# Performance work log

Hardware: AMD Instinct MI355X
Metric: run time of the kernel (lower is better)

The kernel has to match this reference:

```python
import jax, jax.numpy as jnp
import numpy as np

L, B, D, H, LAYERS = 512, 256, 512, 512, 2


def setup_inputs() -> dict:
    key = jax.random.key(0)
    ks = jax.random.split(key, 7)
    s = 0.05  # small init scale for stable recurrence
    return {
        "carry": jnp.zeros((B, LAYERS * H), jnp.float32),
        "x": jax.random.normal(ks[0], (L, B, D), jnp.float32),
        "Wi0": jax.random.normal(ks[1], (D, 3 * H), jnp.float32) * s,
        "Wh0": jax.random.normal(ks[2], (H, 3 * H), jnp.float32) * s,
        "bh0": jnp.zeros((3 * H,), jnp.float32),
        "Wi1": jax.random.normal(ks[3], (H, 3 * H), jnp.float32) * s,
        "Wh1": jax.random.normal(ks[4], (H, 3 * H), jnp.float32) * s,
        "bh1": jnp.zeros((3 * H,), jnp.float32),
    }


def _gru_cell(h, xin, Wi, Wh, bh):
    # flax.linen.GRUCell math: input-side Dense has no bias, hidden-side Dense has bias.
    gi = xin @ Wi            # [B, 3H] -> (ir, iz, in)
    gh = h @ Wh + bh         # [B, 3H] -> (hr, hz, hn)
    ir, iz, inn = jnp.split(gi, 3, axis=-1)
    hr, hz, hn = jnp.split(gh, 3, axis=-1)
    r = jax.nn.sigmoid(ir + hr)
    z = jax.nn.sigmoid(iz + hz)
    n = jnp.tanh(inn + r * hn)
    return (1.0 - z) * n + z * h


def reference(carry, x, Wi0, Wh0, bh0, Wi1, Wh1, bh1):
    params = ((Wi0, Wh0, bh0), (Wi1, Wh1, bh1))

    def step(c, xt):
        hs = jnp.split(c, LAYERS, axis=-1)  # per-layer hidden states
        inp = xt
        new_hs = []
        for i, (Wi, Wh, bh) in enumerate(params):  # fixed small layer loop
            h = _gru_cell(hs[i], inp, Wi, Wh, bh)
            new_hs.append(h)
            inp = h  # output of layer i feeds layer i+1
        return jnp.concatenate(new_hs, axis=-1), inp

    carry, y = jax.lax.scan(step, carry, x)  # y: [L, B, H]
    return carry, y
```

## Files before the change

### kernel.cpp

```cpp
#include <hip/hip_runtime.h>


#define LSEQ 512
#define TH3 1536

#define WT_OFF   0
#define H0_OFF   6291456
#define H1_OFF   6815744
#define BAR_OFF  7340032

typedef _Float16 f16x8 __attribute__((ext_vector_type(8)));
typedef float f32x4 __attribute__((ext_vector_type(4)));

__device__ __forceinline__ float sig_(float v) { return 1.0f / (1.0f + __expf(-v)); }
__device__ __forceinline__ float tanh_(float v) { return 2.0f / (1.0f + __expf(-2.0f * v)) - 1.0f; }

__device__ __forceinline__ f32x4 load16_bypass(const void* p) {
  f32x4 r;
  asm volatile("global_load_dwordx4 %0, %1, off sc0 sc1" : "=v"(r) : "v"(p));
  return r;
}
__device__ __forceinline__ void store2_bypass(_Float16* p, _Float16 v) {
  asm volatile("global_store_short %0, %1, off sc0 sc1" :: "v"(p), "v"(v) : "memory");
}

__global__ void prep_kernel(const float* __restrict__ Wh0, const float* __restrict__ Wi1,
                            const float* __restrict__ Wh1, const float* __restrict__ Wi0,
                            char* __restrict__ ws) {
  const int b = blockIdx.x;
  const int w = b >> 9;
  const int k = b & 511;
  const float* src = (w == 0) ? Wh0 : (w == 1) ? Wi1 : (w == 2) ? Wh1 : Wi0;
  _Float16* dst = (_Float16*)(ws + WT_OFF);
  const int kc = k >> 5;
  const int lthi = ((k >> 3) & 3) << 4;
  const int e = k & 7;
  for (int col = threadIdx.x; col < TH3; col += 256) {
    float v = src[(size_t)k * TH3 + col];
    int nt = col >> 9, c = col & 511, cid = c >> 4, j = c & 15;
    size_t idx = (size_t)(w * 32 + cid) * 24576 + (size_t)((kc * 3 + nt) * 64 + lthi + j) * 8 + e;
    dst[idx] = (_Float16)v;
  }
  if (b == 0) {
    unsigned int* bar = (unsigned int*)(ws + BAR_OFF);
    for (int i = threadIdx.x; i < 512; i += 256) bar[i] = 0u;
  }
}

__device__ __forceinline__ void group_barrier(unsigned int* bar) {
  __syncthreads();
  if (threadIdx.x == 0) {
    unsigned int my = __hip_atomic_load(bar + 1, __ATOMIC_RELAXED, __HIP_MEMORY_SCOPE_AGENT);
    unsigned int prev = __hip_atomic_fetch_add(bar, 1u, __ATOMIC_RELAXED, __HIP_MEMORY_SCOPE_AGENT);
    if (prev == 31u) {
      __hip_atomic_store(bar, 0u, __ATOMIC_RELAXED, __HIP_MEMORY_SCOPE_AGENT);
      __hip_atomic_fetch_add(bar + 1, 1u, __ATOMIC_RELAXED, __HIP_MEMORY_SCOPE_AGENT);
    } else {
      while (__hip_atomic_load(bar + 1, __ATOMIC_RELAXED, __HIP_MEMORY_SCOPE_AGENT) == my) {
      }
    }
  }
  __syncthreads();
}

__global__ void __launch_bounds__(512, 2)
gru_kernel(const float* __restrict__ carry, const float* __restrict__ x,
           const float* __restrict__ bh0, const float* __restrict__ bh1,
           float* __restrict__ out, char* __restrict__ ws) {
  extern __shared__ char smem[];
  _Float16* Wlds = (_Float16*)smem;
  float* GH = (float*)(smem + 147456);

  const int bid = blockIdx.x;
  const int g = bid & 7, cid = bid >> 3;
  const int tid = threadIdx.x;
  const int wid = tid >> 6, lane = tid & 63;
  const int l16 = lane & 15, lhi = lane >> 4;
  const int mhalf = wid & 1, role = wid >> 1;

  _Float16* wt = (_Float16*)(ws + WT_OFF);
  _Float16* h0buf = (_Float16*)(ws + H0_OFF) + (size_t)g * 32768;
  _Float16* h1buf = (_Float16*)(ws + H1_OFF) + (size_t)g * 32768;
  unsigned int* bar = (unsigned int*)(ws + BAR_OFF) + g * 64;

  for (int w = 0; w < 3; ++w) {
    const f16x8* s8 = (const f16x8*)(wt + (size_t)(w * 32 + cid) * 24576);
    f16x8* d8 = (f16x8*)(Wlds + w * 24576);
    for (int i = tid; i < 3072; i += 512) d8[i] = s8[i];
  }

  const int hcol = cid * 16 + l16;
  const int rowq0 = mhalf * 16 + 4 * lhi;

  float bR = 0.f, bZ = 0.f, bN = 0.f;
  f32x4 hst = {0.f, 0.f, 0.f, 0.f};
  if (role == 1 || role == 2) {
    const float* bh = (role == 1) ? bh0 : bh1;
    bR = bh[hcol]; bZ = bh[512 + hcol]; bN = bh[1024 + hcol];
    const int loff = (role == 1) ? 0 : 512;
    _Float16* hb = (role == 1) ? h0buf : h1buf;
#pragma unroll
    for (int q = 0; q < 4; ++q) {
      float h = carry[(size_t)(g * 32 + rowq0 + q) * 1024 + loff + hcol];
      hst[q] = h;
      store2_bypass(&hb[16384 + (rowq0 + q) * 512 + hcol], (_Float16)h);
    }
    asm volatile("s_waitcnt vmcnt(0)" ::: "memory");
  }
  group_barrier(bar);

  const f16x8* Wb0 = (const f16x8*)Wlds;
  const f16x8* Wb1 = (const f16x8*)(Wlds + 24576);
  const f16x8* Wb2 = (const f16x8*)(Wlds + 2 * 24576);
  const f16x8* WbX = (const f16x8*)(wt + (size_t)(3 * 32 + cid) * 24576);

  for (int s = 0; s <= LSEQ; ++s) {
    const int pr = (s + 1) & 1;
    const int pw = s & 1;
    f32x4 a0 = {0.f, 0.f, 0.f, 0.f}, a1 = {0.f, 0.f, 0.f, 0.f}, a2 = {0.f, 0.f, 0.f, 0.f};

    if (role == 0 && s < LSEQ) {
      const _Float16* Ap = h0buf + pr * 16384 + (mhalf * 16 + l16) * 512 + 8 * lhi;
      f16x8 afr[16];
#pragma unroll
      for (int kc = 0; kc < 16; ++kc) afr[kc] = __builtin_bit_cast(f16x8, load16_bypass(Ap + kc * 32));
      asm volatile("s_waitcnt vmcnt(0)" ::: "memory");
      __builtin_amdgcn_sched_barrier(0);
#pragma unroll
      for (int kc = 0; kc < 16; ++kc) {
        a0 = __builtin_amdgcn_mfma_f32_16x16x32_f16(afr[kc], Wb0[(kc * 3 + 0) * 64 + lane], a0, 0, 0, 0);
        a1 = __builtin_amdgcn_mfma_f32_16x16x32_f16(afr[kc], Wb0[(kc * 3 + 1) * 64 + lane], a1, 0, 0, 0);
        a2 = __builtin_amdgcn_mfma_f32_16x16x32_f16(afr[kc], Wb0[(kc * 3 + 2) * 64 + lane], a2, 0, 0, 0);
      }
#pragma unroll
      for (int q = 0; q < 4; ++q) {
        GH[(0 * 32 + rowq0 + q) * 16 + l16] = a0[q];
        GH[(1 * 32 + rowq0 + q) * 16 + l16] = a1[q];
        GH[(2 * 32 + rowq0 + q) * 16 + l16] = a2[q];
      }
    } else if (role == 3 && s >= 1) {
      const _Float16* Ap = h1buf + pw * 16384 + (mhalf * 16 + l16) * 512 + 8 * lhi;
      f16x8 afr[16];
#pragma unroll
      for (int kc = 0; kc < 16; ++kc) afr[kc] = __builtin_bit_cast(f16x8, load16_bypass(Ap + kc * 32));
      asm volatile("s_waitcnt vmcnt(0)" ::: "memory");
      __builtin_amdgcn_sched_barrier(0);
#pragma unroll
      for (int kc = 0; kc < 16; ++kc) {
        a0 = __builtin_amdgcn_mfma_f32_16x16x32_f16(afr[kc], Wb2[(kc * 3 + 0) * 64 + lane], a0, 0, 0, 0);
        a1 = __builtin_amdgcn_mfma_f32_16x16x32_f16(afr[kc], Wb2[(kc * 3 + 1) * 64 + lane], a1, 0, 0, 0);
        a2 = __builtin_amdgcn_mfma_f32_16x16x32_f16(afr[kc], Wb2[(kc * 3 + 2) * 64 + lane], a2, 0, 0, 0);
      }
#pragma unroll
      for (int q = 0; q < 4; ++q) {
        GH[((3 + 0) * 32 + rowq0 + q) * 16 + l16] = a0[q];
        GH[((3 + 1) * 32 + rowq0 + q) * 16 + l16] = a1[q];
        GH[((3 + 2) * 32 + rowq0 + q) * 16 + l16] = a2[q];
      }
    } else if (role == 1 && s < LSEQ) {
      const float* xp = x + ((size_t)s * 256 + g * 32 + mhalf * 16 + l16) * 512 + 8 * lhi;
#pragma unroll
      for (int kc = 0; kc < 16; ++kc) {
        f32x4 xa = *(const f32x4*)(xp + kc * 32);
        f32x4 xb = *(const f32x4*)(xp + kc * 32 + 4);
        f16x8 a;
        a[0] = (_Float16)xa[0]; a[1] = (_Float16)xa[1]; a[2] = (_Float16)xa[2]; a[3] = (_Float16)xa[3];
        a[4] = (_Float16)xb[0]; a[5] = (_Float16)xb[1]; a[6] = (_Float16)xb[2]; a[7] = (_Float16)xb[3];
        a0 = __builtin_amdgcn_mfma_f32_16x16x32_f16(a, WbX[(kc * 3 + 0) * 64 + lane], a0, 0, 0, 0);
        a1 = __builtin_amdgcn_mfma_f32_16x16x32_f16(a, WbX[(kc * 3 + 1) * 64 + lane], a1, 0, 0, 0);
        a2 = __builtin_amdgcn_mfma_f32_16x16x32_f16(a, WbX[(kc * 3 + 2) * 64 + lane], a2, 0, 0, 0);
      }
    } else if (role == 2 && s >= 1) {
      const _Float16* Ap = h0buf + pr * 16384 + (mhalf * 16 + l16) * 512 + 8 * lhi;
      f16x8 afr[16];
#pragma unroll
      for (int kc = 0; kc < 16; ++kc) afr[kc] = __builtin_bit_cast(f16x8, load16_bypass(Ap + kc * 32));
      asm volatile("s_waitcnt vmcnt(0)" ::: "memory");
      __builtin_amdgcn_sched_barrier(0);
#pragma unroll
      for (int kc = 0; kc < 16; ++kc) {
        a0 = __builtin_amdgcn_mfma_f32_16x16x32_f16(afr[kc], Wb1[(kc * 3 + 0) * 64 + lane], a0, 0, 0, 0);
        a1 = __builtin_amdgcn_mfma_f32_16x16x32_f16(afr[kc], Wb1[(kc * 3 + 1) * 64 + lane], a1, 0, 0, 0);
        a2 = __builtin_amdgcn_mfma_f32_16x16x32_f16(afr[kc], Wb1[(kc * 3 + 2) * 64 + lane], a2, 0, 0, 0);
      }
    }
    __syncthreads();

    if (role == 1 && s < LSEQ) {
#pragma unroll
      for (int q = 0; q < 4; ++q) {
        const int row = rowq0 + q;
        float r = sig_(a0[q] + GH[(0 * 32 + row) * 16 + l16] + bR);
        float z = sig_(a1[q] + GH[(1 * 32 + row) * 16 + l16] + bZ);
        float n = tanh_(a2[q] + r * (GH[(2 * 32 + row) * 16 + l16] + bN));
        float h = (1.0f - z) * n + z * hst[q];
        hst[q] = h;
        store2_bypass(&h0buf[pw * 16384 + row * 512 + hcol], (_Float16)h);
        if (s == LSEQ - 1) out[(size_t)(g * 32 + row) * 1024 + hcol] = h;
      }
      asm volatile("s_waitcnt vmcnt(0)" ::: "memory");
    } else if (role == 2 && s >= 1) {
#pragma unroll
      for (int q = 0; q < 4; ++q) {
        const int row = rowq0 + q;
        float r = sig_(a0[q] + GH[((3 + 0) * 32 + row) * 16 + l16] + bR);
        float z = sig_(a1[q] + GH[((3 + 1) * 32 + row) * 16 + l16] + bZ);
        float n = tanh_(a2[q] + r * (GH[((3 + 2) * 32 + row) * 16 + l16] + bN));
        float h = (1.0f - z) * n + z * hst[q];
        hst[q] = h;
        store2_bypass(&h1buf[pr * 16384 + row * 512 + hcol], (_Float16)h);
        out[(size_t)262144 + ((size_t)(s - 1) * 256 + g * 32 + row) * 512 + hcol] = h;
        if (s == LSEQ) out[(size_t)(g * 32 + row) * 1024 + 512 + hcol] = h;
      }
      asm volatile("s_waitcnt vmcnt(0)" ::: "memory");
    }
    group_barrier(bar);
  }
}

extern "C" void kernel_launch(void* const* d_in, const int* in_sizes, int n_in,
                              void* d_out, int out_size, void* d_ws, size_t ws_size,
                              hipStream_t stream) {
  const float* carry = (const float*)d_in[0];
  const float* x     = (const float*)d_in[1];
  const float* Wi0   = (const float*)d_in[2];
  const float* Wh0   = (const float*)d_in[3];
  const float* bh0   = (const float*)d_in[4];
  const float* Wi1   = (const float*)d_in[5];
  const float* Wh1   = (const float*)d_in[6];
  const float* bh1   = (const float*)d_in[7];
  float* out = (float*)d_out;
  char* ws = (char*)d_ws;

  prep_kernel<<<2048, 256, 0, stream>>>(Wh0, Wi1, Wh1, Wi0, ws);

  (void)hipFuncSetAttribute(reinterpret_cast<const void*>(gru_kernel),
                            hipFuncAttributeMaxDynamicSharedMemorySize, 159744);

  void* args[] = {(void*)&carry, (void*)&x, (void*)&bh0, (void*)&bh1, (void*)&out, (void*)&ws};
  (void)hipLaunchCooperativeKernel(reinterpret_cast<void*>(gru_kernel),
                                   dim3(256), dim3(512), args, 159744, stream);
}
```

Measured before the change: 9.717 ms.

## Map batch groups to XCCs at runtime so h-exchange can stay in L2

Each block reads its hardware XCC id and takes a rank within that XCC through atomics, so every batch group of 32 blocks lands on one XCC. When the mapping is valid, the hidden-state loads and stores drop the sc1 bit and can be served from the XCC-local L2 instead of bypassing to memory. If the mapping check fails, the kernel falls back to the old block-index mapping with full bypass. The group barrier is also simplified to a monotonically increasing counter. This adds a two-phase global startup barrier across all 256 blocks, which relies on every block being co-resident.

```diff
diff --git a/kernel.cpp b/kernel.cpp
--- a/kernel.cpp
+++ b/kernel.cpp
@@ -8,6 +8,9 @@
 #define H0_OFF   6291456
 #define H1_OFF   6815744
 #define BAR_OFF  7340032
+#define RANK_OFF 7342080
+#define GBAR_OFF 7344128
+#define BAD_OFF  7344384
 
 typedef _Float16 f16x8 __attribute__((ext_vector_type(8)));
 typedef float f32x4 __attribute__((ext_vector_type(4)));
@@ -15,13 +18,17 @@
 __device__ __forceinline__ float sig_(float v) { return 1.0f / (1.0f + __expf(-v)); }
 __device__ __forceinline__ float tanh_(float v) { return 2.0f / (1.0f + __expf(-2.0f * v)) - 1.0f; }
 
-__device__ __forceinline__ f32x4 load16_bypass(const void* p) {
+template <bool FAST>
+__device__ __forceinline__ f32x4 load16h(const void* p) {
   f32x4 r;
-  asm volatile("global_load_dwordx4 %0, %1, off sc0 sc1" : "=v"(r) : "v"(p));
+  if (FAST) asm volatile("global_load_dwordx4 %0, %1, off sc0" : "=v"(r) : "v"(p));
+  else      asm volatile("global_load_dwordx4 %0, %1, off sc0 sc1" : "=v"(r) : "v"(p));
   return r;
 }
-__device__ __forceinline__ void store2_bypass(_Float16* p, _Float16 v) {
-  asm volatile("global_store_short %0, %1, off sc0 sc1" :: "v"(p), "v"(v) : "memory");
+template <bool FAST>
+__device__ __forceinline__ void store2h(_Float16* p, _Float16 v) {
+  if (FAST) asm volatile("global_store_short %0, %1, off sc0" :: "v"(p), "v"(v) : "memory");
+  else      asm volatile("global_store_short %0, %1, off sc0 sc1" :: "v"(p), "v"(v) : "memory");
 }
 
 __global__ void prep_kernel(const float* __restrict__ Wh0, const float* __restrict__ Wi1,
@@ -42,37 +49,24 @@
     dst[idx] = (_Float16)v;
   }
   if (b == 0) {
-    unsigned int* bar = (unsigned int*)(ws + BAR_OFF);
-    for (int i = threadIdx.x; i < 512; i += 256) bar[i] = 0u;
-  }
-}
-
-__device__ __forceinline__ void group_barrier(unsigned int* bar) {
+    unsigned int* z = (unsigned int*)(ws + BAR_OFF);
+    for (int i = threadIdx.x; i < 1152; i += 256) z[i] = 0u;
+  }
+}
+
+__device__ __forceinline__ void group_barrier(unsigned int* barp, unsigned int target, int tid) {
   __syncthreads();
-  if (threadIdx.x == 0) {
-    unsigned int my = __hip_atomic_load(bar + 1, __ATOMIC_RELAXED, __HIP_MEMORY_SCOPE_AGENT);
-    unsigned int prev = __hip_atomic_fetch_add(bar, 1u, __ATOMIC_RELAXED, __HIP_MEMORY_SCOPE_AGENT);
-    if (prev == 31u) {
-      __hip_atomic_store(bar, 0u, __ATOMIC_RELAXED, __HIP_MEMORY_SCOPE_AGENT);
-      __hip_atomic_fetch_add(bar + 1, 1u, __ATOMIC_RELAXED, __HIP_MEMORY_SCOPE_AGENT);
-    } else {
-      while (__hip_atomic_load(bar + 1, __ATOMIC_RELAXED, __HIP_MEMORY_SCOPE_AGENT) == my) {
-      }
-    }
+  if (tid == 0) {
+    __hip_atomic_fetch_add(barp, 1u, __ATOMIC_RELAXED, __HIP_MEMORY_SCOPE_AGENT);
+    while (__hip_atomic_load(barp, __ATOMIC_RELAXED, __HIP_MEMORY_SCOPE_AGENT) < target) {}
   }
   __syncthreads();
 }
 
-__global__ void __launch_bounds__(512, 2)
-gru_kernel(const float* __restrict__ carry, const float* __restrict__ x,
-           const float* __restrict__ bh0, const float* __restrict__ bh1,
-           float* __restrict__ out, char* __restrict__ ws) {
-  extern __shared__ char smem[];
-  _Float16* Wlds = (_Float16*)smem;
-  float* GH = (float*)(smem + 147456);
-
-  const int bid = blockIdx.x;
-  const int g = bid & 7, cid = bid >> 3;
+template <bool FAST>
+__device__ __forceinline__ void run_scan(int g, int cid, const float* carry, const float* x,
+                                         const float* bh0, const float* bh1, float* out,
+                                         char* ws, _Float16* Wlds, float* GH) {
   const int tid = threadIdx.x;
   const int wid = tid >> 6, lane = tid & 63;
   const int l16 = lane & 15, lhi = lane >> 4;
@@ -81,13 +75,8 @@
   _Float16* wt = (_Float16*)(ws + WT_OFF);
   _Float16* h0buf = (_Float16*)(ws + H0_OFF) + (size_t)g * 32768;
   _Float16* h1buf = (_Float16*)(ws + H1_OFF) + (size_t)g * 32768;
-  unsigned int* bar = (unsigned int*)(ws + BAR_OFF) + g * 64;
-
-  for (int w = 0; w < 3; ++w) {
-    const f16x8* s8 = (const f16x8*)(wt + (size_t)(w * 32 + cid) * 24576);
-    f16x8* d8 = (f16x8*)(Wlds + w * 24576);
-    for (int i = tid; i < 3072; i += 512) d8[i] = s8[i];
-  }
+  unsigned int* barp = (unsigned int*)(ws + BAR_OFF) + g * 64;
+  unsigned int phase = 0;
 
   const int hcol = cid * 16 + l16;
   const int rowq0 = mhalf * 16 + 4 * lhi;
@@ -103,11 +92,11 @@
     for (int q = 0; q < 4; ++q) {
       float h = carry[(size_t)(g * 32 + rowq0 + q) * 1024 + loff + hcol];
       hst[q] = h;
-      store2_bypass(&hb[16384 + (rowq0 + q) * 512 + hcol], (_Float16)h);
+      store2h<FAST>(&hb[16384 + (rowq0 + q) * 512 + hcol], (_Float16)h);
     }
     asm volatile("s_waitcnt vmcnt(0)" ::: "memory");
   }
-  group_barrier(bar);
+  group_barrier(barp, 32u * (++phase), tid);
 
   const f16x8* Wb0 = (const f16x8*)Wlds;
   const f16x8* Wb1 = (const f16x8*)(Wlds + 24576);
@@ -123,7 +112,7 @@
       const _Float16* Ap = h0buf + pr * 16384 + (mhalf * 16 + l16) * 512 + 8 * lhi;
       f16x8 afr[16];
 #pragma unroll
-      for (int kc = 0; kc < 16; ++kc) afr[kc] = __builtin_bit_cast(f16x8, load16_bypass(Ap + kc * 32));
+      for (int kc = 0; kc < 16; ++kc) afr[kc] = __builtin_bit_cast(f16x8, load16h<FAST>(Ap + kc * 32));
       asm volatile("s_waitcnt vmcnt(0)" ::: "memory");
       __builtin_amdgcn_sched_barrier(0);
 #pragma unroll
@@ -142,7 +131,7 @@
       const _Float16* Ap = h1buf + pw * 16384 + (mhalf * 16 + l16) * 512 + 8 * lhi;
       f16x8 afr[16];
 #pragma unroll
-      for (int kc = 0; kc < 16; ++kc) afr[kc] = __builtin_bit_cast(f16x8, load16_bypass(Ap + kc * 32));
+      for (int kc = 0; kc < 16; ++kc) afr[kc] = __builtin_bit_cast(f16x8, load16h<FAST>(Ap + kc * 32));
       asm volatile("s_waitcnt vmcnt(0)" ::: "memory");
       __builtin_amdgcn_sched_barrier(0);
 #pragma unroll
@@ -174,7 +163,7 @@
       const _Float16* Ap = h0buf + pr * 16384 + (mhalf * 16 + l16) * 512 + 8 * lhi;
       f16x8 afr[16];
 #pragma unroll
-      for (int kc = 0; kc < 16; ++kc) afr[kc] = __builtin_bit_cast(f16x8, load16_bypass(Ap + kc * 32));
+      for (int kc = 0; kc < 16; ++kc) afr[kc] = __builtin_bit_cast(f16x8, load16h<FAST>(Ap + kc * 32));
       asm volatile("s_waitcnt vmcnt(0)" ::: "memory");
       __builtin_amdgcn_sched_barrier(0);
 #pragma unroll
@@ -195,7 +184,7 @@
         float n = tanh_(a2[q] + r * (GH[(2 * 32 + row) * 16 + l16] + bN));
         float h = (1.0f - z) * n + z * hst[q];
         hst[q] = h;
-        store2_bypass(&h0buf[pw * 16384 + row * 512 + hcol], (_Float16)h);
+        store2h<FAST>(&h0buf[pw * 16384 + row * 512 + hcol], (_Float16)h);
         if (s == LSEQ - 1) out[(size_t)(g * 32 + row) * 1024 + hcol] = h;
       }
       asm volatile("s_waitcnt vmcnt(0)" ::: "memory");
@@ -208,14 +197,61 @@
         float n = tanh_(a2[q] + r * (GH[((3 + 2) * 32 + row) * 16 + l16] + bN));
         float h = (1.0f - z) * n + z * hst[q];
         hst[q] = h;
-        store2_bypass(&h1buf[pr * 16384 + row * 512 + hcol], (_Float16)h);
+        store2h<FAST>(&h1buf[pr * 16384 + row * 512 + hcol], (_Float16)h);
         out[(size_t)262144 + ((size_t)(s - 1) * 256 + g * 32 + row) * 512 + hcol] = h;
         if (s == LSEQ) out[(size_t)(g * 32 + row) * 1024 + 512 + hcol] = h;
       }
       asm volatile("s_waitcnt vmcnt(0)" ::: "memory");
     }
-    group_barrier(bar);
-  }
+    group_barrier(barp, 32u * (++phase), tid);
+  }
+}
+
+__global__ void __launch_bounds__(512, 2)
+gru_kernel(const float* __restrict__ carry, const float* __restrict__ x,
+           const float* __restrict__ bh0, const float* __restrict__ bh1,
+           float* __restrict__ out, char* __restrict__ ws) {
+  extern __shared__ char smem[];
+  _Float16* Wlds = (_Float16*)smem;
+  float* GH = (float*)(smem + 147456);
+  __shared__ int sh_g, sh_cid, sh_fast;
+
+  const int tid = threadIdx.x;
+
+  if (tid == 0) {
+    unsigned int xcc;
+    asm volatile("s_getreg_b32 %0, hwreg(HW_REG_XCC_ID)" : "=s"(xcc));
+    xcc &= 7u;
+    unsigned int* rk = (unsigned int*)(ws + RANK_OFF) + xcc * 64;
+    unsigned int* gb = (unsigned int*)(ws + GBAR_OFF);
+    unsigned int* bd = (unsigned int*)(ws + BAD_OFF);
+    unsigned int cid_raw = __hip_atomic_fetch_add(rk, 1u, __ATOMIC_RELAXED, __HIP_MEMORY_SCOPE_AGENT);
+    asm volatile("s_waitcnt vmcnt(0)" ::: "memory");
+    __hip_atomic_fetch_add(gb, 1u, __ATOMIC_RELAXED, __HIP_MEMORY_SCOPE_AGENT);
+    while (__hip_atomic_load(gb, __ATOMIC_RELAXED, __HIP_MEMORY_SCOPE_AGENT) < 256u) {}
+    unsigned int cnt = __hip_atomic_load(rk, __ATOMIC_RELAXED, __HIP_MEMORY_SCOPE_AGENT);
+    if (cnt != 32u || cid_raw >= 32u)
+      __hip_atomic_fetch_add(bd, 1u, __ATOMIC_RELAXED, __HIP_MEMORY_SCOPE_AGENT);
+    asm volatile("s_waitcnt vmcnt(0)" ::: "memory");
+    __hip_atomic_fetch_add(gb, 1u, __ATOMIC_RELAXED, __HIP_MEMORY_SCOPE_AGENT);
+    while (__hip_atomic_load(gb, __ATOMIC_RELAXED, __HIP_MEMORY_SCOPE_AGENT) < 512u) {}
+    unsigned int badv = __hip_atomic_load(bd, __ATOMIC_RELAXED, __HIP_MEMORY_SCOPE_AGENT);
+    sh_fast = (badv == 0u);
+    sh_g    = (badv == 0u) ? (int)xcc     : (int)(blockIdx.x & 7);
+    sh_cid  = (badv == 0u) ? (int)cid_raw : (int)(blockIdx.x >> 3);
+  }
+  __syncthreads();
+  const int g = sh_g, cid = sh_cid;
+
+  _Float16* wt = (_Float16*)(ws + WT_OFF);
+  for (int w = 0; w < 3; ++w) {
+    const f16x8* s8 = (const f16x8*)(wt + (size_t)(w * 32 + cid) * 24576);
+    f16x8* d8 = (f16x8*)(Wlds + w * 24576);
+    for (int i = tid; i < 3072; i += 512) d8[i] = s8[i];
+  }
+
+  if (sh_fast) run_scan<true>(g, cid, carry, x, bh0, bh1, out, ws, Wlds, GH);
+  else         run_scan<false>(g, cid, carry, x, bh0, bh1, out, ws, Wlds, GH);
 }
 
 extern "C" void kernel_launch(void* const* d_in, const int* in_sizes, int n_in,
```

New measurement: 8.616 ms. 11.3% less time.

## Replace per-step group barrier with per-wave dataflow flags and LDS handoffs

Applied to the files above, without the earlier changes.

Removes the block-wide __syncthreads plus single-thread atomic group barrier that ran every timestep. Each wave role now runs its own loop and synchronises through per-wave global flags, polled with a 64-lane ballot, and LDS release/acquire counters. This lets layer-0 and layer-1 work and the x-projection run ahead of each other instead of moving in lockstep. The cost is more global polling traffic and a subtle memory-ordering protocol that relies on relaxed atomics and cache-bypass stores being visible across blocks.

```diff
diff --git a/kernel.cpp b/kernel.cpp
--- a/kernel.cpp
+++ b/kernel.cpp
@@ -7,7 +7,8 @@
 #define WT_OFF   0
 #define H0_OFF   6291456
 #define H1_OFF   6815744
-#define BAR_OFF  7340032
+#define F0_OFF   7340032
+#define F1_OFF   7405568
 
 typedef _Float16 f16x8 __attribute__((ext_vector_type(8)));
 typedef float f32x4 __attribute__((ext_vector_type(4)));
@@ -15,13 +16,30 @@
 __device__ __forceinline__ float sig_(float v) { return 1.0f / (1.0f + __expf(-v)); }
 __device__ __forceinline__ float tanh_(float v) { return 2.0f / (1.0f + __expf(-2.0f * v)) - 1.0f; }
 
-__device__ __forceinline__ f32x4 load16_bypass(const void* p) {
+__device__ __forceinline__ f32x4 load16b(const void* p) {
   f32x4 r;
   asm volatile("global_load_dwordx4 %0, %1, off sc0 sc1" : "=v"(r) : "v"(p));
   return r;
 }
-__device__ __forceinline__ void store2_bypass(_Float16* p, _Float16 v) {
+__device__ __forceinline__ void store2b(_Float16* p, _Float16 v) {
   asm volatile("global_store_short %0, %1, off sc0 sc1" :: "v"(p), "v"(v) : "memory");
+}
+
+__device__ __forceinline__ void astore(unsigned int* p, unsigned int v) {
+  __hip_atomic_store(p, v, __ATOMIC_RELAXED, __HIP_MEMORY_SCOPE_AGENT);
+}
+__device__ __forceinline__ unsigned int aload(unsigned int* p) {
+  return __hip_atomic_load(p, __ATOMIC_RELAXED, __HIP_MEMORY_SCOPE_AGENT);
+}
+__device__ __forceinline__ void poll64(char* base, int lane, unsigned int target) {
+  unsigned int* p = (unsigned int*)(base + lane * 128);
+  while (__ballot(aload(p) >= target) != ~0ull) {}
+}
+__device__ __forceinline__ void lds_post(unsigned int* f, unsigned int v) {
+  __hip_atomic_store(f, v, __ATOMIC_RELEASE, __HIP_MEMORY_SCOPE_WORKGROUP);
+}
+__device__ __forceinline__ void lds_poll(unsigned int* f, unsigned int v) {
+  while (__hip_atomic_load(f, __ATOMIC_ACQUIRE, __HIP_MEMORY_SCOPE_WORKGROUP) < v) {}
 }
 
 __global__ void prep_kernel(const float* __restrict__ Wh0, const float* __restrict__ Wi1,
@@ -42,25 +60,9 @@
     dst[idx] = (_Float16)v;
   }
   if (b == 0) {
-    unsigned int* bar = (unsigned int*)(ws + BAR_OFF);
-    for (int i = threadIdx.x; i < 512; i += 256) bar[i] = 0u;
-  }
-}
-
-__device__ __forceinline__ void group_barrier(unsigned int* bar) {
-  __syncthreads();
-  if (threadIdx.x == 0) {
-    unsigned int my = __hip_atomic_load(bar + 1, __ATOMIC_RELAXED, __HIP_MEMORY_SCOPE_AGENT);
-    unsigned int prev = __hip_atomic_fetch_add(bar, 1u, __ATOMIC_RELAXED, __HIP_MEMORY_SCOPE_AGENT);
-    if (prev == 31u) {
-      __hip_atomic_store(bar, 0u, __ATOMIC_RELAXED, __HIP_MEMORY_SCOPE_AGENT);
-      __hip_atomic_fetch_add(bar + 1, 1u, __ATOMIC_RELAXED, __HIP_MEMORY_SCOPE_AGENT);
-    } else {
-      while (__hip_atomic_load(bar + 1, __ATOMIC_RELAXED, __HIP_MEMORY_SCOPE_AGENT) == my) {
-      }
-    }
-  }
-  __syncthreads();
+    unsigned int* z = (unsigned int*)(ws + F0_OFF);
+    for (int i = threadIdx.x; i < 32768; i += 256) z[i] = 0u;
+  }
 }
 
 __global__ void __launch_bounds__(512, 2)
@@ -69,152 +71,197 @@
            float* __restrict__ out, char* __restrict__ ws) {
   extern __shared__ char smem[];
   _Float16* Wlds = (_Float16*)smem;
-  float* GH = (float*)(smem + 147456);
-
-  const int bid = blockIdx.x;
-  const int g = bid & 7, cid = bid >> 3;
+  float* gi0buf = (float*)(smem + 147456);
+  float* gh1buf = (float*)(smem + 153600);
+  __shared__ unsigned int sf[8];
+
   const int tid = threadIdx.x;
   const int wid = tid >> 6, lane = tid & 63;
   const int l16 = lane & 15, lhi = lane >> 4;
   const int mhalf = wid & 1, role = wid >> 1;
+  const int g = blockIdx.x & 7, cid = blockIdx.x >> 3;
+
+  if (tid < 8) sf[tid] = 0u;
 
   _Float16* wt = (_Float16*)(ws + WT_OFF);
   _Float16* h0buf = (_Float16*)(ws + H0_OFF) + (size_t)g * 32768;
   _Float16* h1buf = (_Float16*)(ws + H1_OFF) + (size_t)g * 32768;
-  unsigned int* bar = (unsigned int*)(ws + BAR_OFF) + g * 64;
+  char* f0g = ws + F0_OFF + (size_t)g * 64 * 128;
+  char* f1g = ws + F1_OFF + (size_t)g * 64 * 128;
+  unsigned int* myf0 = (unsigned int*)(f0g + (cid * 2 + mhalf) * 128);
+  unsigned int* myf1 = (unsigned int*)(f1g + (cid * 2 + mhalf) * 128);
 
   for (int w = 0; w < 3; ++w) {
     const f16x8* s8 = (const f16x8*)(wt + (size_t)(w * 32 + cid) * 24576);
     f16x8* d8 = (f16x8*)(Wlds + w * 24576);
     for (int i = tid; i < 3072; i += 512) d8[i] = s8[i];
   }
-
-  const int hcol = cid * 16 + l16;
-  const int rowq0 = mhalf * 16 + 4 * lhi;
-
-  float bR = 0.f, bZ = 0.f, bN = 0.f;
-  f32x4 hst = {0.f, 0.f, 0.f, 0.f};
-  if (role == 1 || role == 2) {
-    const float* bh = (role == 1) ? bh0 : bh1;
-    bR = bh[hcol]; bZ = bh[512 + hcol]; bN = bh[1024 + hcol];
-    const int loff = (role == 1) ? 0 : 512;
-    _Float16* hb = (role == 1) ? h0buf : h1buf;
-#pragma unroll
-    for (int q = 0; q < 4; ++q) {
-      float h = carry[(size_t)(g * 32 + rowq0 + q) * 1024 + loff + hcol];
-      hst[q] = h;
-      store2_bypass(&hb[16384 + (rowq0 + q) * 512 + hcol], (_Float16)h);
-    }
-    asm volatile("s_waitcnt vmcnt(0)" ::: "memory");
-  }
-  group_barrier(bar);
+  __syncthreads();
 
   const f16x8* Wb0 = (const f16x8*)Wlds;
   const f16x8* Wb1 = (const f16x8*)(Wlds + 24576);
   const f16x8* Wb2 = (const f16x8*)(Wlds + 2 * 24576);
   const f16x8* WbX = (const f16x8*)(wt + (size_t)(3 * 32 + cid) * 24576);
 
-  for (int s = 0; s <= LSEQ; ++s) {
-    const int pr = (s + 1) & 1;
-    const int pw = s & 1;
-    f32x4 a0 = {0.f, 0.f, 0.f, 0.f}, a1 = {0.f, 0.f, 0.f, 0.f}, a2 = {0.f, 0.f, 0.f, 0.f};
-
-    if (role == 0 && s < LSEQ) {
-      const _Float16* Ap = h0buf + pr * 16384 + (mhalf * 16 + l16) * 512 + 8 * lhi;
+  const int hcol = cid * 16 + l16;
+  const int rowq0 = mhalf * 16 + 4 * lhi;
+
+  if (role == 0) {
+    float bR = bh0[hcol], bZ = bh0[512 + hcol], bN = bh0[1024 + hcol];
+    f32x4 hst;
+#pragma unroll
+    for (int q = 0; q < 4; ++q) {
+      float h = carry[(size_t)(g * 32 + rowq0 + q) * 1024 + hcol];
+      hst[q] = h;
+      store2b(&h0buf[16384 + (rowq0 + q) * 512 + hcol], (_Float16)h);
+    }
+    asm volatile("s_waitcnt vmcnt(0)" ::: "memory");
+    if (lane == 0) astore(myf0, 1u);
+    for (int t = 0; t < LSEQ; ++t) {
+      poll64(f0g, lane, (unsigned)(t + 1));
+      const _Float16* Ap = h0buf + ((t + 1) & 1) * 16384 + (mhalf * 16 + l16) * 512 + 8 * lhi;
       f16x8 afr[16];
 #pragma unroll
-      for (int kc = 0; kc < 16; ++kc) afr[kc] = __builtin_bit_cast(f16x8, load16_bypass(Ap + kc * 32));
+      for (int kc = 0; kc < 16; ++kc) afr[kc] = __builtin_bit_cast(f16x8, load16b(Ap + kc * 32));
       asm volatile("s_waitcnt vmcnt(0)" ::: "memory");
       __builtin_amdgcn_sched_barrier(0);
-#pragma unroll
-      for (int kc = 0; kc < 16; ++kc) {
-        a0 = __builtin_amdgcn_mfma_f32_16x16x32_f16(afr[kc], Wb0[(kc * 3 + 0) * 64 + lane], a0, 0, 0, 0);
-        a1 = __builtin_amdgcn_mfma_f32_16x16x32_f16(afr[kc], Wb0[(kc * 3 + 1) * 64 + lane], a1, 0, 0, 0);
-        a2 = __builtin_amdgcn_mfma_f32_16x16x32_f16(afr[kc], Wb0[(kc * 3 + 2) * 64 + lane], a2, 0, 0, 0);
-      }
-#pragma unroll
-      for (int q = 0; q < 4; ++q) {
-        GH[(0 * 32 + rowq0 + q) * 16 + l16] = a0[q];
-        GH[(1 * 32 + rowq0 + q) * 16 + l16] = a1[q];
-        GH[(2 * 32 + rowq0 + q) * 16 + l16] = a2[q];
-      }
-    } else if (role == 3 && s >= 1) {
-      const _Float16* Ap = h1buf + pw * 16384 + (mhalf * 16 + l16) * 512 + 8 * lhi;
-      f16x8 afr[16];
-#pragma unroll
-      for (int kc = 0; kc < 16; ++kc) afr[kc] = __builtin_bit_cast(f16x8, load16_bypass(Ap + kc * 32));
-      asm volatile("s_waitcnt vmcnt(0)" ::: "memory");
-      __builtin_amdgcn_sched_barrier(0);
-#pragma unroll
-      for (int kc = 0; kc < 16; ++kc) {
-        a0 = __builtin_amdgcn_mfma_f32_16x16x32_f16(afr[kc], Wb2[(kc * 3 + 0) * 64 + lane], a0, 0, 0, 0);
-        a1 = __builtin_amdgcn_mfma_f32_16x16x32_f16(afr[kc], Wb2[(kc * 3 + 1) * 64 + lane], a1, 0, 0, 0);
-        a2 = __builtin_amdgcn_mfma_f32_16x16x32_f16(afr[kc], Wb2[(kc * 3 + 2) * 64 + lane], a2, 0, 0, 0);
-      }
-#pragma unroll
-      for (int q = 0; q < 4; ++q) {
-        GH[((3 + 0) * 32 + rowq0 + q) * 16 + l16] = a0[q];
-        GH[((3 + 1) * 32 + rowq0 + q) * 16 + l16] = a1[q];
-        GH[((3 + 2) * 32 + rowq0 + q) * 16 + l16] = a2[q];
-      }
-    } else if (role == 1 && s < LSEQ) {
-      const float* xp = x + ((size_t)s * 256 + g * 32 + mhalf * 16 + l16) * 512 + 8 * lhi;
+      f32x4 a0 = {0,0,0,0}, a1 = {0,0,0,0}, a2 = {0,0,0,0};
+#pragma unroll
+      for (int kc = 0; kc < 16; ++kc) {
+        a0 = __builtin_amdgcn_mfma_f32_16x16x32_f16(afr[kc], Wb0[(kc*3+0)*64+lane], a0, 0,0,0);
+        a1 = __builtin_amdgcn_mfma_f32_16x16x32_f16(afr[kc], Wb0[(kc*3+1)*64+lane], a1, 0,0,0);
+        a2 = __builtin_amdgcn_mfma_f32_16x16x32_f16(afr[kc], Wb0[(kc*3+2)*64+lane], a2, 0,0,0);
+      }
+      lds_poll(&sf[0 + mhalf], (unsigned)(t + 1));
+      float hnew[4];
+#pragma unroll
+      for (int q = 0; q < 4; ++q) {
+        const int row = rowq0 + q;
+        float giR = gi0buf[(0*32 + row)*16 + l16];
+        float giZ = gi0buf[(1*32 + row)*16 + l16];
+        float giN = gi0buf[(2*32 + row)*16 + l16];
+        float r = sig_(giR + a0[q] + bR);
+        float z = sig_(giZ + a1[q] + bZ);
+        float n = tanh_(giN + r * (a2[q] + bN));
+        hnew[q] = (1.0f - z) * n + z * hst[q];
+        hst[q] = hnew[q];
+      }
+      poll64(f1g, lane, (unsigned)t);
+#pragma unroll
+      for (int q = 0; q < 4; ++q)
+        store2b(&h0buf[(t & 1) * 16384 + (rowq0 + q) * 512 + hcol], (_Float16)hnew[q]);
+      asm volatile("s_waitcnt vmcnt(0)" ::: "memory");
+      if (lane == 0) astore(myf0, (unsigned)(t + 2));
+      if (lane == 0) lds_post(&sf[2 + mhalf], (unsigned)(t + 1));
+    }
+#pragma unroll
+    for (int q = 0; q < 4; ++q)
+      out[(size_t)(g * 32 + rowq0 + q) * 1024 + hcol] = hst[q];
+  } else if (role == 1) {
+    for (int t = 0; t < LSEQ; ++t) {
+      const float* xp = x + ((size_t)t * 256 + g * 32 + mhalf * 16 + l16) * 512 + 8 * lhi;
+      f32x4 a0 = {0,0,0,0}, a1 = {0,0,0,0}, a2 = {0,0,0,0};
 #pragma unroll
       for (int kc = 0; kc < 16; ++kc) {
         f32x4 xa = *(const f32x4*)(xp + kc * 32);
         f32x4 xb = *(const f32x4*)(xp + kc * 32 + 4);
         f16x8 a;
-        a[0] = (_Float16)xa[0]; a[1] = (_Float16)xa[1]; a[2] = (_Float16)xa[2]; a[3] = (_Float16)xa[3];
-        a[4] = (_Float16)xb[0]; a[5] = (_Float16)xb[1]; a[6] = (_Float16)xb[2]; a[7] = (_Float16)xb[3];
-        a0 = __builtin_amdgcn_mfma_f32_16x16x32_f16(a, WbX[(kc * 3 + 0) * 64 + lane], a0, 0, 0, 0);
-        a1 = __builtin_amdgcn_mfma_f32_16x16x32_f16(a, WbX[(kc * 3 + 1) * 64 + lane], a1, 0, 0, 0);
-        a2 = __builtin_amdgcn_mfma_f32_16x16x32_f16(a, WbX[(kc * 3 + 2) * 64 + lane], a2, 0, 0, 0);
-      }
-    } else if (role == 2 && s >= 1) {
-      const _Float16* Ap = h0buf + pr * 16384 + (mhalf * 16 + l16) * 512 + 8 * lhi;
+        a[0]=(_Float16)xa[0]; a[1]=(_Float16)xa[1]; a[2]=(_Float16)xa[2]; a[3]=(_Float16)xa[3];
+        a[4]=(_Float16)xb[0]; a[5]=(_Float16)xb[1]; a[6]=(_Float16)xb[2]; a[7]=(_Float16)xb[3];
+        a0 = __builtin_amdgcn_mfma_f32_16x16x32_f16(a, WbX[(kc*3+0)*64+lane], a0, 0,0,0);
+        a1 = __builtin_amdgcn_mfma_f32_16x16x32_f16(a, WbX[(kc*3+1)*64+lane], a1, 0,0,0);
+        a2 = __builtin_amdgcn_mfma_f32_16x16x32_f16(a, WbX[(kc*3+2)*64+lane], a2, 0,0,0);
+      }
+      lds_poll(&sf[2 + mhalf], (unsigned)t);
+#pragma unroll
+      for (int q = 0; q < 4; ++q) {
+        const int row = rowq0 + q;
+        gi0buf[(0*32 + row)*16 + l16] = a0[q];
+        gi0buf[(1*32 + row)*16 + l16] = a1[q];
+        gi0buf[(2*32 + row)*16 + l16] = a2[q];
+      }
+      if (lane == 0) lds_post(&sf[0 + mhalf], (unsigned)(t + 1));
+    }
+  } else if (role == 2) {
+    float bR = bh1[hcol], bZ = bh1[512 + hcol], bN = bh1[1024 + hcol];
+    f32x4 hst;
+#pragma unroll
+    for (int q = 0; q < 4; ++q) {
+      float h = carry[(size_t)(g * 32 + rowq0 + q) * 1024 + 512 + hcol];
+      hst[q] = h;
+      store2b(&h1buf[16384 + (rowq0 + q) * 512 + hcol], (_Float16)h);
+    }
+    asm volatile("s_waitcnt vmcnt(0)" ::: "memory");
+    if (lane == 0) astore(myf1, 1u);
+    for (int t = 0; t < LSEQ; ++t) {
+      poll64(f0g, lane, (unsigned)(t + 2));
+      const _Float16* Ap = h0buf + (t & 1) * 16384 + (mhalf * 16 + l16) * 512 + 8 * lhi;
       f16x8 afr[16];
 #pragma unroll
-      for (int kc = 0; kc < 16; ++kc) afr[kc] = __builtin_bit_cast(f16x8, load16_bypass(Ap + kc * 32));
+      for (int kc = 0; kc < 16; ++kc) afr[kc] = __builtin_bit_cast(f16x8, load16b(Ap + kc * 32));
       asm volatile("s_waitcnt vmcnt(0)" ::: "memory");
       __builtin_amdgcn_sched_barrier(0);
-#pragma unroll
-      for (int kc = 0; kc < 16; ++kc) {
-        a0 = __builtin_amdgcn_mfma_f32_16x16x32_f16(afr[kc], Wb1[(kc * 3 + 0) * 64 + lane], a0, 0, 0, 0);
-        a1 = __builtin_amdgcn_mfma_f32_16x16x32_f16(afr[kc], Wb1[(kc * 3 + 1) * 64 + lane], a1, 0, 0, 0);
-        a2 = __builtin_amdgcn_mfma_f32_16x16x32_f16(afr[kc], Wb1[(kc * 3 + 2) * 64 + lane], a2, 0, 0, 0);
-      }
-    }
-    __syncthreads();
-
-    if (role == 1 && s < LSEQ) {
-#pragma unroll
-      for (int q = 0; q < 4; ++q) {
-        const int row = rowq0 + q;
-        float r = sig_(a0[q] + GH[(0 * 32 + row) * 16 + l16] + bR);
-        float z = sig_(a1[q] + GH[(1 * 32 + row) * 16 + l16] + bZ);
-        float n = tanh_(a2[q] + r * (GH[(2 * 32 + row) * 16 + l16] + bN));
-        float h = (1.0f - z) * n + z * hst[q];
-        hst[q] = h;
-        store2_bypass(&h0buf[pw * 16384 + row * 512 + hcol], (_Float16)h);
-        if (s == LSEQ - 1) out[(size_t)(g * 32 + row) * 1024 + hcol] = h;
-      }
-      asm volatile("s_waitcnt vmcnt(0)" ::: "memory");
-    } else if (role == 2 && s >= 1) {
-#pragma unroll
-      for (int q = 0; q < 4; ++q) {
-        const int row = rowq0 + q;
-        float r = sig_(a0[q] + GH[((3 + 0) * 32 + row) * 16 + l16] + bR);
-        float z = sig_(a1[q] + GH[((3 + 1) * 32 + row) * 16 + l16] + bZ);
-        float n = tanh_(a2[q] + r * (GH[((3 + 2) * 32 + row) * 16 + l16] + bN));
-        float h = (1.0f - z) * n + z * hst[q];
-        hst[q] = h;
-        store2_bypass(&h1buf[pr * 16384 + row * 512 + hcol], (_Float16)h);
-        out[(size_t)262144 + ((size_t)(s - 1) * 256 + g * 32 + row) * 512 + hcol] = h;
-        if (s == LSEQ) out[(size_t)(g * 32 + row) * 1024 + 512 + hcol] = h;
-      }
-      asm volatile("s_waitcnt vmcnt(0)" ::: "memory");
-    }
-    group_barrier(bar);
+      f32x4 a0 = {0,0,0,0}, a1 = {0,0,0,0}, a2 = {0,0,0,0};
+#pragma unroll
+      for (int kc = 0; kc < 16; ++kc) {
+        a0 = __builtin_amdgcn_mfma_f32_16x16x32_f16(afr[kc], Wb1[(kc*3+0)*64+lane], a0, 0,0,0);
+        a1 = __builtin_amdgcn_mfma_f32_16x16x32_f16(afr[kc], Wb1[(kc*3+1)*64+lane], a1, 0,0,0);
+        a2 = __builtin_amdgcn_mfma_f32_16x16x32_f16(afr[kc], Wb1[(kc*3+2)*64+lane], a2, 0,0,0);
+      }
+      lds_poll(&sf[4 + mhalf], (unsigned)(t + 1));
+      float hnew[4];
+#pragma unroll
+      for (int q = 0; q < 4; ++q) {
+        const int row = rowq0 + q;
+        float ghR = gh1buf[(0*32 + row)*16 + l16];
+        float ghZ = gh1buf[(1*32 + row)*16 + l16];
+        float ghN = gh1buf[(2*32 + row)*16 + l16];
+        float r = sig_(a0[q] + ghR + bR);
+        float z = sig_(a1[q] + ghZ + bZ);
+        float n = tanh_(a2[q] + r * (ghN + bN));
+        hnew[q] = (1.0f - z) * n + z * hst[q];
+        hst[q] = hnew[q];
+      }
+      poll64(f1g, lane, (unsigned)(t + 1));
+#pragma unroll
+      for (int q = 0; q < 4; ++q)
+        store2b(&h1buf[(t & 1) * 16384 + (rowq0 + q) * 512 + hcol], (_Float16)hnew[q]);
+      asm volatile("s_waitcnt vmcnt(0)" ::: "memory");
+      if (lane == 0) astore(myf1, (unsigned)(t + 2));
+      if (lane == 0) lds_post(&sf[6 + mhalf], (unsigned)(t + 1));
+#pragma unroll
+      for (int q = 0; q < 4; ++q)
+        out[(size_t)262144 + ((size_t)t * 256 + g * 32 + rowq0 + q) * 512 + hcol] = hnew[q];
+    }
+#pragma unroll
+    for (int q = 0; q < 4; ++q)
+      out[(size_t)(g * 32 + rowq0 + q) * 1024 + 512 + hcol] = hst[q];
+  } else {
+    for (int t = 0; t < LSEQ; ++t) {
+      poll64(f1g, lane, (unsigned)(t + 1));
+      const _Float16* Ap = h1buf + ((t + 1) & 1) * 16384 + (mhalf * 16 + l16) * 512 + 8 * lhi;
+      f16x8 afr[16];
+#pragma unroll
+      for (int kc = 0; kc < 16; ++kc) afr[kc] = __builtin_bit_cast(f16x8, load16b(Ap + kc * 32));
+      asm volatile("s_waitcnt vmcnt(0)" ::: "memory");
+      __builtin_amdgcn_sched_barrier(0);
+      f32x4 a0 = {0,0,0,0}, a1 = {0,0,0,0}, a2 = {0,0,0,0};
+#pragma unroll
+      for (int kc = 0; kc < 16; ++kc) {
+        a0 = __builtin_amdgcn_mfma_f32_16x16x32_f16(afr[kc], Wb2[(kc*3+0)*64+lane], a0, 0,0,0);
+        a1 = __builtin_amdgcn_mfma_f32_16x16x32_f16(afr[kc], Wb2[(kc*3+1)*64+lane], a1, 0,0,0);
+        a2 = __builtin_amdgcn_mfma_f32_16x16x32_f16(afr[kc], Wb2[(kc*3+2)*64+lane], a2, 0,0,0);
+      }
+      lds_poll(&sf[6 + mhalf], (unsigned)t);
+#pragma unroll
+      for (int q = 0; q < 4; ++q) {
+        const int row = rowq0 + q;
+        gh1buf[(0*32 + row)*16 + l16] = a0[q];
+        gh1buf[(1*32 + row)*16 + l16] = a1[q];
+        gh1buf[(2*32 + row)*16 + l16] = a2[q];
+      }
+      if (lane == 0) lds_post(&sf[4 + mhalf], (unsigned)(t + 1));
+    }
   }
 }
 
```

New measurement: 17.96 ms. 84.9% more time.
